# Kernel tuning notes

Hardware: AMD Instinct MI355X
Metric: run time of the kernel (lower is better)

## Reference

```python
import jax, jax.numpy as jnp
import numpy as np

HEADS, OUT_C = 8, 16
NEG_SLOPE = 0.2  # PyG GATConv default negative_slope


def setup_inputs() -> dict:
    key = jax.random.key(0)
    ks = jax.random.split(key, 6)
    N, E, IN = 100000, 1600000, 128
    x = jax.random.normal(ks[0], (N, IN), jnp.float32)
    edge_index = jax.random.randint(ks[1], (2, E), 0, N, dtype=jnp.int32)
    W = jax.random.normal(ks[2], (IN, HEADS * OUT_C), jnp.float32) / np.float32(np.sqrt(IN))
    att_src = jax.random.normal(ks[3], (HEADS, OUT_C), jnp.float32) * 0.1
    att_dst = jax.random.normal(ks[4], (HEADS, OUT_C), jnp.float32) * 0.1
    bias = jax.random.normal(ks[5], (HEADS * OUT_C,), jnp.float32) * 0.01
    return {"x": x, "edge_index": edge_index, "W": W,
            "att_src": att_src, "att_dst": att_dst, "bias": bias}


def reference(x, edge_index, W, att_src, att_dst, bias):
    N = x.shape[0]
    # Linear projection, split into heads: [N, H, C]
    xw = (x @ W).reshape(N, HEADS, OUT_C)
    # Add self-loops (PyG default add_self_loops=True)
    loops = jnp.arange(N, dtype=edge_index.dtype)
    src = jnp.concatenate([edge_index[0], loops])
    dst = jnp.concatenate([edge_index[1], loops])
    # Per-node attention terms [N, H], then per-edge logits
    a_s = jnp.einsum('nhc,hc->nh', xw, att_src)
    a_d = jnp.einsum('nhc,hc->nh', xw, att_dst)
    e = a_s[src] + a_d[dst]                       # [Etot, H]
    e = jnp.where(e > 0, e, NEG_SLOPE * e)        # LeakyReLU
    # Segment softmax over edges grouped by destination node
    emax = jax.ops.segment_max(e, dst, num_segments=N)
    p = jnp.exp(e - emax[dst])
    denom = jax.ops.segment_sum(p, dst, num_segments=N)
    alpha = p / (denom[dst] + 1e-16)              # [Etot, H]
    # Weighted scatter-aggregate of source messages
    out = jax.ops.segment_sum(xw[src] * alpha[:, :, None], dst, num_segments=N)
    out = out.reshape(N, HEADS * OUT_C) + bias    # concat heads + bias
    return jax.nn.relu(out)                       # act='relu', norm=None
```

## Files before the change

### kernel.cpp

```cpp
#include <hip/hip_runtime.h>
#include <math.h>

#define HEADS 8
#define OUTC 16
#define HC 128
#define NEG_SLOPE 0.2f
#define LOG2E 1.44269504f

#define BM 128
#define BK 32
#define XPAD 132
#define CAP 64

typedef unsigned int uint;
typedef unsigned short ushort;

__device__ __forceinline__ ushort f2bf(float f) {
    uint u = __float_as_uint(f);
    u += 0x7FFFu + ((u >> 16) & 1u);
    return (ushort)(u >> 16);
}

__global__ __launch_bounds__(256, 4) void k_fused(
    const float* __restrict__ x, const float* __restrict__ W,
    const float* __restrict__ att_src, const float* __restrict__ att_dst,
    const int* __restrict__ ei,
    ushort* __restrict__ xwh, float* __restrict__ a_s, float* __restrict__ a_d,
    int* __restrict__ deg, int* __restrict__ csr,
    int N, int E, int GB) {
    __shared__ float xs[BK][XPAD];
    __shared__ float Ws[BK][XPAD];

    if (blockIdx.x >= GB) {
        int e = (blockIdx.x - GB) * 256 + threadIdx.x;
        if (e < E) {
            int src = ei[e];
            int dst = ei[E + e];
            int slot = atomicAdd(&deg[dst], 1);
            if (slot < CAP) csr[(size_t)dst * CAP + slot] = src;
        }
        return;
    }

    int t = threadIdx.x;
    int nb0 = blockIdx.x * BM;
    int tc = t & 15;
    int tr = t >> 4;

    float acc[8][8];
#pragma unroll
    for (int i = 0; i < 8; ++i)
#pragma unroll
        for (int j = 0; j < 8; ++j) acc[i][j] = 0.0f;

    for (int k0 = 0; k0 < HC; k0 += BK) {
        int kk4 = (t & 7) * 4;
#pragma unroll
        for (int p = 0; p < 4; ++p) {
            int nr = (t >> 3) + p * 32;
            int node = nb0 + nr;
            float4 v = make_float4(0.f, 0.f, 0.f, 0.f);
            if (node < N) v = *(const float4*)&x[(size_t)node * HC + k0 + kk4];
            xs[kk4 + 0][nr] = v.x;
            xs[kk4 + 1][nr] = v.y;
            xs[kk4 + 2][nr] = v.z;
            xs[kk4 + 3][nr] = v.w;
        }
        int kk = t >> 3;
        int c4 = (t & 7) * 4;
#pragma unroll
        for (int j = 0; j < 4; ++j) {
            *(float4*)&Ws[kk][c4 + j * 32] =
                *(const float4*)&W[(size_t)(k0 + kk) * HC + c4 + j * 32];
        }
        __syncthreads();

#pragma unroll 4
        for (int k = 0; k < BK; ++k) {
            float xa[8], wa[8];
            *(float4*)&xa[0] = *(const float4*)&xs[k][tr * 8];
            *(float4*)&xa[4] = *(const float4*)&xs[k][tr * 8 + 4];
            *(float4*)&wa[0] = *(const float4*)&Ws[k][tc * 8];
            *(float4*)&wa[4] = *(const float4*)&Ws[k][tc * 8 + 4];
#pragma unroll
            for (int i = 0; i < 8; ++i)
#pragma unroll
                for (int j = 0; j < 8; ++j)
                    acc[i][j] = fmaf(xa[i], wa[j], acc[i][j]);
        }
        __syncthreads();
    }

    float as8[8], ad8[8];
#pragma unroll
    for (int j = 0; j < 8; ++j) {
        as8[j] = att_src[tc * 8 + j];
        ad8[j] = att_dst[tc * 8 + j];
    }
    int h = tc >> 1;
#pragma unroll
    for (int i = 0; i < 8; ++i) {
        int node = nb0 + tr * 8 + i;
        float vs = 0.f, vd = 0.f;
        ushort h8[8];
#pragma unroll
        for (int j = 0; j < 8; ++j) {
            vs = fmaf(acc[i][j], as8[j], vs);
            vd = fmaf(acc[i][j], ad8[j], vd);
            h8[j] = f2bf(acc[i][j]);
        }
        vs += __shfl_xor(vs, 1);
        vd += __shfl_xor(vd, 1);
        if (node < N) {
            *(uint4*)&xwh[(size_t)node * HC + tc * 8] = *(uint4*)&h8[0];
            if ((tc & 1) == 0) {
                a_s[node * HEADS + h] = vs * LOG2E;
                a_d[node * HEADS + h] = vd * LOG2E;
            }
        }
    }
}

__global__ __launch_bounds__(256) void k_node(
    const int* __restrict__ deg, const int* __restrict__ csr,
    const float* __restrict__ a_s, const float* __restrict__ a_d,
    const uint* __restrict__ xwh, const float* __restrict__ bias,
    float* __restrict__ out, int N) {
    int wave = blockIdx.x * 4 + (threadIdx.x >> 6);
    int n0 = wave * 2;
    if (n0 >= N) return;
    int n1 = n0 + 1;
    bool has1 = (n1 < N);
    int l = threadIdx.x & 63;
    int hB = l >> 3;

    float adn0 = a_d[n0 * HEADS + hB];
    float adn1 = has1 ? a_d[n1 * HEADS + hB] : 0.0f;

    float v0 = a_s[n0 * HEADS + hB] + adn0;
    v0 = v0 > 0.0f ? v0 : NEG_SLOPE * v0;
    float p0 = exp2f(v0);
    float den0 = p0;
    uint t0 = xwh[n0 * 64 + l];
    float a00 = p0 * __uint_as_float(t0 << 16);
    float a01 = p0 * __uint_as_float(t0 & 0xFFFF0000u);

    float den1 = 0.0f, a10 = 0.0f, a11 = 0.0f;
    if (has1) {
        float v1 = a_s[n1 * HEADS + hB] + adn1;
        v1 = v1 > 0.0f ? v1 : NEG_SLOPE * v1;
        float p1 = exp2f(v1);
        den1 = p1;
        uint t1 = xwh[n1 * 64 + l];
        a10 = p1 * __uint_as_float(t1 << 16);
        a11 = p1 * __uint_as_float(t1 & 0xFFFF0000u);
    }

    int cnt0 = deg[n0]; if (cnt0 > CAP) cnt0 = CAP;
    int cnt1 = has1 ? deg[n1] : 0; if (cnt1 > CAP) cnt1 = CAP;
    const int* row0 = csr + (size_t)n0 * CAP;
    const int* row1 = csr + (size_t)n1 * CAP;
    int cmax = cnt0 > cnt1 ? cnt0 : cnt1;

    for (int base = 0; base < cmax; base += 4) {
        int s0[4], s1[4];
#pragma unroll
        for (int j = 0; j < 4; ++j) {
            int i = base + j;
            s0[j] = (i < cnt0) ? row0[i] : -1;
            s1[j] = (i < cnt1) ? row1[i] : -1;
        }
        float as0[4], as1[4];
        uint w0[4], w1[4];
#pragma unroll
        for (int j = 0; j < 4; ++j) {
            if (s0[j] >= 0) {
                as0[j] = a_s[s0[j] * HEADS + hB];
                w0[j]  = xwh[(size_t)s0[j] * 64 + l];
            }
            if (s1[j] >= 0) {
                as1[j] = a_s[s1[j] * HEADS + hB];
                w1[j]  = xwh[(size_t)s1[j] * 64 + l];
            }
        }
#pragma unroll
        for (int j = 0; j < 4; ++j) {
            if (s0[j] >= 0) {
                float v = as0[j] + adn0;
                v = v > 0.0f ? v : NEG_SLOPE * v;
                float p = exp2f(v);
                den0 += p;
                a00 = fmaf(p, __uint_as_float(w0[j] << 16), a00);
                a01 = fmaf(p, __uint_as_float(w0[j] & 0xFFFF0000u), a01);
            }
            if (s1[j] >= 0) {
                float v = as1[j] + adn1;
                v = v > 0.0f ? v : NEG_SLOPE * v;
                float p = exp2f(v);
                den1 += p;
                a10 = fmaf(p, __uint_as_float(w1[j] << 16), a10);
                a11 = fmaf(p, __uint_as_float(w1[j] & 0xFFFF0000u), a11);
            }
        }
    }

    float2 b = *(const float2*)&bias[2 * l];
    {
        float inv = 1.0f / (den0 + 1e-16f);
        float r0 = a00 * inv + b.x;
        float r1 = a01 * inv + b.y;
        float2 o;
        o.x = r0 > 0.0f ? r0 : 0.0f;
        o.y = r1 > 0.0f ? r1 : 0.0f;
        *(float2*)&out[(size_t)n0 * HC + 2 * l] = o;
    }
    if (has1) {
        float inv = 1.0f / (den1 + 1e-16f);
        float r0 = a10 * inv + b.x;
        float r1 = a11 * inv + b.y;
        float2 o;
        o.x = r0 > 0.0f ? r0 : 0.0f;
        o.y = r1 > 0.0f ? r1 : 0.0f;
        *(float2*)&out[(size_t)n1 * HC + 2 * l] = o;
    }
}

extern "C" void kernel_launch(void* const* d_in, const int* in_sizes, int n_in,
                              void* d_out, int out_size, void* d_ws, size_t ws_size,
                              hipStream_t stream) {
    const float* x       = (const float*)d_in[0];
    const int*   ei      = (const int*)d_in[1];
    const float* W       = (const float*)d_in[2];
    const float* att_src = (const float*)d_in[3];
    const float* att_dst = (const float*)d_in[4];
    const float* bias    = (const float*)d_in[5];
    float* out = (float*)d_out;

    int N = in_sizes[0] / HC;
    int E = in_sizes[1] / 2;

    ushort* xwh = (ushort*)d_ws;
    float* a_s  = (float*)(xwh + (size_t)N * HC);
    float* a_d  = a_s + (size_t)N * HEADS;
    int* deg    = (int*)(a_d + (size_t)N * HEADS);
    int* csr    = deg + N;

    hipMemsetAsync(deg, 0, (size_t)N * sizeof(int), stream);

    int GB = (N + BM - 1) / BM;
    int SB = (E + 255) / 256;
    k_fused<<<GB + SB, 256, 0, stream>>>(x, W, att_src, att_dst, ei,
                                         xwh, a_s, a_d, deg, csr, N, E, GB);

    int waves = (N + 1) / 2;
    k_node<<<(waves + 3) / 4, 256, 0, stream>>>(deg, csr, a_s, a_d,
                                                (const uint*)xwh, bias, out, N);
}
```

Measured before the change: 290.9 us.

## Partition CSR scatter by destination range and add nontemporal load/store hints

The edge-scatter blocks now each take a 2048-edge chunk, and every chunk is processed by 8 blocks. Each of those blocks only performs the atomic increment and CSR write for destinations in its own eighth of the node range. The aim is to keep each block's atomics and CSR writes in a narrower address window for better cache locality. The cost is that edge_index is read eight times and most loaded edges are filtered out. Separately, the x loads, edge loads and bf16 xw stores use nontemporal builtins to reduce cache pollution.

```diff
diff --git a/kernel.cpp b/kernel.cpp
--- a/kernel.cpp
+++ b/kernel.cpp
@@ -11,9 +11,13 @@
 #define BK 32
 #define XPAD 132
 #define CAP 64
+#define CHUNK 2048
 
 typedef unsigned int uint;
 typedef unsigned short ushort;
+typedef float  __attribute__((ext_vector_type(4))) f32x4;
+typedef int    __attribute__((ext_vector_type(4))) i32x4;
+typedef uint   __attribute__((ext_vector_type(4))) u32x4;
 
 __device__ __forceinline__ ushort f2bf(float f) {
     uint u = __float_as_uint(f);
@@ -31,19 +35,54 @@
     __shared__ float xs[BK][XPAD];
     __shared__ float Ws[BK][XPAD];
 
-    if (blockIdx.x >= GB) {
-        int e = (blockIdx.x - GB) * 256 + threadIdx.x;
-        if (e < E) {
-            int src = ei[e];
-            int dst = ei[E + e];
-            int slot = atomicAdd(&deg[dst], 1);
-            if (slot < CAP) csr[(size_t)dst * CAP + slot] = src;
+    int bid = blockIdx.x;
+    if (bid >= GB) {
+        int i = bid - GB;
+        int chunk = i >> 3;
+        int r = bid & 7;
+        int R8 = (N + 7) >> 3;
+        int lo = r * R8;
+        int hi = lo + R8; if (hi > N) hi = N;
+
+        int cbase = chunk * CHUNK;
+        int t = threadIdx.x;
+        int srcs[8], dsts[8];
+#pragma unroll
+        for (int g = 0; g < 2; ++g) {
+            int e = cbase + g * 1024 + 4 * t;
+            if (e + 3 < E) {
+                i32x4 s4 = __builtin_nontemporal_load((const i32x4*)&ei[e]);
+                i32x4 d4 = __builtin_nontemporal_load((const i32x4*)&ei[E + e]);
+                srcs[4 * g + 0] = s4.x; srcs[4 * g + 1] = s4.y;
+                srcs[4 * g + 2] = s4.z; srcs[4 * g + 3] = s4.w;
+                dsts[4 * g + 0] = d4.x; dsts[4 * g + 1] = d4.y;
+                dsts[4 * g + 2] = d4.z; dsts[4 * g + 3] = d4.w;
+            } else {
+#pragma unroll
+                for (int j = 0; j < 4; ++j) {
+                    int ee = e + j;
+                    if (ee < E) {
+                        srcs[4 * g + j] = ei[ee];
+                        dsts[4 * g + j] = ei[E + ee];
+                    } else {
+                        dsts[4 * g + j] = -1;
+                    }
+                }
+            }
+        }
+#pragma unroll
+        for (int k = 0; k < 8; ++k) {
+            int d = dsts[k];
+            if (d >= lo && d < hi) {
+                int slot = atomicAdd(&deg[d], 1);
+                if (slot < CAP) csr[(size_t)d * CAP + slot] = srcs[k];
+            }
         }
         return;
     }
 
     int t = threadIdx.x;
-    int nb0 = blockIdx.x * BM;
+    int nb0 = bid * BM;
     int tc = t & 15;
     int tr = t >> 4;
 
@@ -59,8 +98,9 @@
         for (int p = 0; p < 4; ++p) {
             int nr = (t >> 3) + p * 32;
             int node = nb0 + nr;
-            float4 v = make_float4(0.f, 0.f, 0.f, 0.f);
-            if (node < N) v = *(const float4*)&x[(size_t)node * HC + k0 + kk4];
+            f32x4 v = {0.f, 0.f, 0.f, 0.f};
+            if (node < N)
+                v = __builtin_nontemporal_load((const f32x4*)&x[(size_t)node * HC + k0 + kk4]);
             xs[kk4 + 0][nr] = v.x;
             xs[kk4 + 1][nr] = v.y;
             xs[kk4 + 2][nr] = v.z;
@@ -112,7 +152,8 @@
         vs += __shfl_xor(vs, 1);
         vd += __shfl_xor(vd, 1);
         if (node < N) {
-            *(uint4*)&xwh[(size_t)node * HC + tc * 8] = *(uint4*)&h8[0];
+            u32x4 hv = *(u32x4*)&h8[0];
+            __builtin_nontemporal_store(hv, (u32x4*)&xwh[(size_t)node * HC + tc * 8]);
             if ((tc & 1) == 0) {
                 a_s[node * HEADS + h] = vs * LOG2E;
                 a_d[node * HEADS + h] = vd * LOG2E;
@@ -248,9 +289,10 @@
     hipMemsetAsync(deg, 0, (size_t)N * sizeof(int), stream);
 
     int GB = (N + BM - 1) / BM;
-    int SB = (E + 255) / 256;
-    k_fused<<<GB + SB, 256, 0, stream>>>(x, W, att_src, att_dst, ei,
-                                         xwh, a_s, a_d, deg, csr, N, E, GB);
+    int SC = (E + CHUNK - 1) / CHUNK;
+    int SBLK = SC * 8;
+    k_fused<<<GB + SBLK, 256, 0, stream>>>(x, W, att_src, att_dst, ei,
+                                           xwh, a_s, a_d, deg, csr, N, E, GB);
 
     int waves = (N + 1) / 2;
     k_node<<<(waves + 3) / 4, 256, 0, stream>>>(deg, csr, a_s, a_d,
```

After: 290.3 us. Within noise of the previous version (-0.2%).
